# Kernel tuning notes

Measured on AMD Instinct MI355X. Metric: run time of the kernel, lower is better.

Reference implementation:

```python
import jax, jax.numpy as jnp
import numpy as np
import math

N_HEADS = 8
EMB = 128
KEY_DIM = EMB // N_HEADS  # 16
B, NQ, T = 32, 1024, 1024


def _uniform(key, shape, stdv):
    return jax.random.uniform(key, shape, jnp.float32, -stdv, stdv)


def setup_inputs() -> dict:
    key = jax.random.key(0)
    ks = jax.random.split(key, 7)
    stdv = 1.0 / math.sqrt(KEY_DIM)      # last dim of w_query/w_key/w_value
    stdv_o = 1.0 / math.sqrt(EMB)        # last dim of w_out
    q = jax.random.normal(ks[0], (B, NQ, EMB), jnp.float32)
    h = jax.random.normal(ks[1], (B, T, EMB), jnp.float32)
    mask = jax.random.randint(ks[2], (B, NQ, T), 0, 2).astype(bool)
    return {
        "q": q,
        "h": h,
        "mask": mask,
        "w_query": _uniform(ks[3], (N_HEADS, EMB, KEY_DIM), stdv),
        "w_key": _uniform(ks[4], (N_HEADS, EMB, KEY_DIM), stdv),
        "w_value": _uniform(ks[5], (N_HEADS, EMB, KEY_DIM), stdv),
        "w_out": _uniform(ks[6], (N_HEADS, KEY_DIM, EMB), stdv_o),
    }


def reference(q, h, mask, w_query, w_key, w_value, w_out):
    # q: [B, NQ, E], h: [B, T, E], mask: [B, NQ, T] (True = blocked)
    scale = 1.0 / math.sqrt(KEY_DIM)
    Q = jnp.einsum('bqi,hik->hbqk', q, w_query)   # [H,B,NQ,dk]
    K = jnp.einsum('bti,hik->hbtk', h, w_key)     # [H,B,T,dk]
    V = jnp.einsum('bti,hiv->hbtv', h, w_value)   # [H,B,T,dv]
    U = scale * jnp.einsum('hbqk,hbtk->hbqt', Q, K)  # [H,B,NQ,T]
    m = mask[None]                                   # broadcast over heads
    U = jnp.where(m, -jnp.inf, U)
    attn = jax.nn.softmax(U, axis=-1)
    attn = jnp.where(m, 0.0, attn)                   # explicit zeroing as in original
    heads = jnp.einsum('hbqt,hbtv->hbqv', attn, V)   # [H,B,NQ,dv]
    out = jnp.einsum('hbqv,hve->bqe', heads, w_out)  # [B,NQ,E]
    return out
```

## Files before the change

kernel.cpp:

```cpp
#include <hip/hip_runtime.h>
#include <hip/hip_bf16.h>
#include <stdint.h>


typedef __attribute__((ext_vector_type(8))) short bf16x8;
typedef __attribute__((ext_vector_type(4))) float f32x4;

#define NEGBIG (-1e30f)
#define QSCALE 0.36067376022224085f
#define EXP2(x) __builtin_amdgcn_exp2f(x)

__device__ __forceinline__ unsigned short f2bf(float x) {
  union { __hip_bfloat16 h; unsigned short u; } cv;
  cv.h = __float2bfloat16(x);
  return cv.u;
}
__device__ __forceinline__ unsigned int pk2bf(float a, float b) {
  unsigned int ua = __float_as_uint(a) + 0x8000u;
  unsigned int ub = __float_as_uint(b) + 0x8000u;
  return __builtin_amdgcn_perm(ub, ua, 0x07060302u);
}

__global__ __launch_bounds__(256) void maskpack_k(const void* __restrict__ mask,
                                                  unsigned long long* __restrict__ mp64) {
  __shared__ unsigned short mlds[256];
  const int tid = threadIdx.x;
  const unsigned int* mi = (const unsigned int*)mask;
  unsigned int acc = 0;
  #pragma unroll
  for (int k = 0; k < 16; ++k) acc |= mi[k * 251];
  const bool bytemode = acc > 1u;

  const long long i0 = ((long long)blockIdx.x * 256 + tid) * 16;
  unsigned int v = 0;
  if (bytemode) {
    int4 w = *(const int4*)((const unsigned char*)mask + i0);
    unsigned int ws[4] = {(unsigned)w.x, (unsigned)w.y, (unsigned)w.z, (unsigned)w.w};
    #pragma unroll
    for (int d = 0; d < 4; ++d)
      #pragma unroll
      for (int j = 0; j < 4; ++j)
        v |= (((ws[d] >> (8*j)) & 0xFFu) ? 1u : 0u) << (d*4 + j);
  } else {
    const int4* mp = (const int4*)((const int*)mask + i0);
    #pragma unroll
    for (int d = 0; d < 4; ++d) {
      int4 w = mp[d];
      v |= (w.x ? 1u : 0u) << (d*4 + 0);
      v |= (w.y ? 1u : 0u) << (d*4 + 1);
      v |= (w.z ? 1u : 0u) << (d*4 + 2);
      v |= (w.w ? 1u : 0u) << (d*4 + 3);
    }
  }
  mlds[tid] = (unsigned short)v;
  __syncthreads();
  if (tid < 64)
    mp64[(long long)blockIdx.x * 64 + tid] = ((const unsigned long long*)mlds)[tid];
}

__global__ __launch_bounds__(256) void projqkv_k(const float* __restrict__ qp,
                                                 const float* __restrict__ hp,
                                                 const float* __restrict__ wqp,
                                                 const float* __restrict__ wkp,
                                                 const float* __restrict__ wvp,
                                                 unsigned short* __restrict__ Qb,
                                                 unsigned short* __restrict__ Kb,
                                                 unsigned short* __restrict__ Vt) {
  __shared__ unsigned short WtLds[128 * 136];
  __shared__ __align__(16) unsigned short Cxf[9216];
  const int tid = threadIdx.x;
  const int wave = tid >> 6, lane = tid & 63;
  const int llo4 = lane & 15, lhi4 = lane >> 4;
  const int m0 = blockIdx.x * 64;
  const int b = m0 >> 10, row0 = m0 & 1023;
  const int sel = blockIdx.y;
  const float* A = (sel == 0) ? qp : hp;
  const float* W = (sel == 0) ? wqp : (sel == 1) ? wkp : wvp;
  const float wscale = (sel == 0) ? QSCALE : 1.0f;

  #pragma unroll
  for (int i = 0; i < 8; ++i) {
    int base = (tid + i * 256) * 8;
    float4 w0 = *(const float4*)&W[base];
    float4 w1 = *(const float4*)&W[base + 4];
    float wv8[8] = {w0.x, w0.y, w0.z, w0.w, w1.x, w1.y, w1.z, w1.w};
    #pragma unroll
    for (int j = 0; j < 8; ++j) {
      int idx = base + j;
      int h = idx >> 11, e = (idx >> 4) & 127, kk = idx & 15;
      WtLds[(h*16 + kk) * 136 + e] = f2bf(wv8[j] * wscale);
    }
  }
  #pragma unroll
  for (int i = 0; i < 4; ++i) {
    int r = (tid >> 4) + i * 16;
    int c = (tid & 15) * 8;
    float4 a0 = *(const float4*)&A[(m0 + r) * 128 + c];
    float4 a1 = *(const float4*)&A[(m0 + r) * 128 + c + 4];
    bf16x8 a8;
    a8[0] = (short)f2bf(a0.x); a8[1] = (short)f2bf(a0.y);
    a8[2] = (short)f2bf(a0.z); a8[3] = (short)f2bf(a0.w);
    a8[4] = (short)f2bf(a1.x); a8[5] = (short)f2bf(a1.y);
    a8[6] = (short)f2bf(a1.z); a8[7] = (short)f2bf(a1.w);
    *(bf16x8*)&Cxf[r * 136 + c] = a8;
  }
  __syncthreads();

  const int n0 = wave * 32;
  f32x4 acc[4][2] = {};
  #pragma unroll
  for (int kk = 0; kk < 128; kk += 32) {
    bf16x8 af[4], bfr[2];
    #pragma unroll
    for (int mi2 = 0; mi2 < 4; ++mi2)
      af[mi2] = *(const bf16x8*)&Cxf[(mi2*16 + llo4)*136 + kk + lhi4*8];
    #pragma unroll
    for (int ni = 0; ni < 2; ++ni)
      bfr[ni] = *(const bf16x8*)&WtLds[(n0 + ni*16 + llo4)*136 + kk + lhi4*8];
    #pragma unroll
    for (int mi2 = 0; mi2 < 4; ++mi2)
      #pragma unroll
      for (int ni = 0; ni < 2; ++ni)
        acc[mi2][ni] = __builtin_amdgcn_mfma_f32_16x16x32_bf16(af[mi2], bfr[ni], acc[mi2][ni], 0, 0, 0);
  }

  __syncthreads();
  if (sel < 2) {
    unsigned short* Cb = sel ? Kb : Qb;
    #pragma unroll
    for (int mi2 = 0; mi2 < 4; ++mi2)
      #pragma unroll
      for (int ni = 0; ni < 2; ++ni) {
        int n = n0 + ni*16 + llo4;
        #pragma unroll
        for (int r = 0; r < 4; ++r)
          Cxf[(mi2*16 + lhi4*4 + r)*136 + n] = f2bf(acc[mi2][ni][r]);
      }
    __syncthreads();
    #pragma unroll
    for (int it = 0; it < 4; ++it) {
      int u = tid + it*256;
      int h = u >> 7, rk = u & 127, row = rk >> 1, kh = rk & 1;
      bf16x8 vv = *(const bf16x8*)&Cxf[row*136 + h*16 + kh*8];
      *(bf16x8*)&Cb[((b*8 + h)*1024 + row0 + row)*16 + kh*8] = vv;
    }
  } else {
    #pragma unroll
    for (int mi2 = 0; mi2 < 4; ++mi2)
      #pragma unroll
      for (int ni = 0; ni < 2; ++ni) {
        int n = n0 + ni*16 + llo4;
        ushort4 pk;
        pk.x = f2bf(acc[mi2][ni][0]); pk.y = f2bf(acc[mi2][ni][1]);
        pk.z = f2bf(acc[mi2][ni][2]); pk.w = f2bf(acc[mi2][ni][3]);
        *(ushort4*)&Cxf[n*72 + mi2*16 + lhi4*4] = pk;
      }
    __syncthreads();
    #pragma unroll
    for (int it = 0; it < 4; ++it) {
      int u = tid + it*256;
      int n = u >> 3, tc = u & 7;
      int h = n >> 4, k = n & 15;
      bf16x8 vv = *(const bf16x8*)&Cxf[n*72 + tc*8];
      *(bf16x8*)&Vt[((b*8 + h)*16 + k)*1024 + row0 + tc*8] = vv;
    }
  }
}

__global__ __launch_bounds__(256) void attn_k(const unsigned short* __restrict__ Qb,
                                              const unsigned short* __restrict__ Kb,
                                              const unsigned short* __restrict__ Vtb,
                                              const unsigned long long* __restrict__ mp64,
                                              unsigned short* __restrict__ heads) {
  __shared__ __align__(16) unsigned short Plds[4][16 * 72];
  const int tid = threadIdx.x;
  const int wave = tid >> 6, lane = tid & 63;
  const int llo4 = lane & 15, lhi4 = lane >> 4;
  const int q0 = blockIdx.x * 64 + wave * 16;
  const int b  = blockIdx.y;
  const int h  = blockIdx.z;
  const int bh = b * 8 + h;
  unsigned short* Pw = &Plds[wave][0];
  const unsigned long long* mrow_p = &mp64[((b << 10) + q0 + llo4) * 16];

  bf16x8 qf = {};
  if (lhi4 < 2)
    qf = *(const bf16x8*)&Qb[(bh * 1024 + q0 + llo4) * 16 + lhi4 * 8];

  bf16x8 kf[4] = {};
  bf16x8 ones;
  #pragma unroll
  for (int j = 0; j < 8; ++j) ones[j] = (short)0x3F80;
  const f32x4 cbias = {-18.f, -18.f, -18.f, -18.f};

  f32x4 ot = {};
  f32x4 lacc = {};

  for (int tw = 0; tw < 16; ++tw) {
    const int t0 = tw * 64;
    if (lhi4 < 2) {
      #pragma unroll
      for (int tt = 0; tt < 4; ++tt)
        kf[tt] = *(const bf16x8*)&Kb[(bh * 1024 + t0 + tt*16 + llo4) * 16 + lhi4 * 8];
    }
    bf16x8 vf[2];
    #pragma unroll
    for (int kt = 0; kt < 2; ++kt)
      vf[kt] = *(const bf16x8*)&Vtb[(bh * 16 + llo4) * 1024 + t0 + kt*32 + lhi4 * 8];
    unsigned long long mw = mrow_p[tw];

    f32x4 st[4];
    #pragma unroll
    for (int tt = 0; tt < 4; ++tt)
      st[tt] = __builtin_amdgcn_mfma_f32_16x16x32_bf16(kf[tt], qf, cbias, 0, 0, 0);

    #pragma unroll
    for (int tt = 0; tt < 4; ++tt) {
      unsigned int msh = (unsigned int)(mw >> (tt*16 + lhi4*4));
      #pragma unroll
      for (int r = 0; r < 4; ++r) {
        float s = ((msh >> r) & 1u) ? NEGBIG : st[tt][r];
        st[tt][r] = EXP2(s);
      }
    }
    #pragma unroll
    for (int tt = 0; tt < 4; ++tt) {
      uint2 d;
      d.x = pk2bf(st[tt][0], st[tt][1]);
      d.y = pk2bf(st[tt][2], st[tt][3]);
      *(uint2*)&Pw[llo4 * 72 + tt*16 + lhi4*4] = d;
    }
    #pragma unroll
    for (int kt = 0; kt < 2; ++kt) {
      bf16x8 pf = *(const bf16x8*)&Pw[llo4 * 72 + kt*32 + lhi4*8];
      ot   = __builtin_amdgcn_mfma_f32_16x16x32_bf16(vf[kt], pf, ot, 0, 0, 0);
      lacc = __builtin_amdgcn_mfma_f32_16x16x32_bf16(ones,  pf, lacc, 0, 0, 0);
    }
  }

  float l = lacc[0];
  float inv = l > 0.f ? 1.f / l : 0.f;
  f32x4 o = ot * inv;
  uint2 d;
  d.x = pk2bf(o[0], o[1]);
  d.y = pk2bf(o[2], o[3]);
  *(uint2*)&heads[((b << 10) + q0 + llo4) * 128 + h*16 + lhi4*4] = d;
}

__global__ __launch_bounds__(256) void outproj_k(const unsigned short* __restrict__ Av,
                                                 const float* __restrict__ W,
                                                 float* __restrict__ Co) {
  __shared__ unsigned short WtLds[128 * 136];
  __shared__ __align__(16) unsigned short Cxf[9216];
  const int tid = threadIdx.x;
  const int wave = tid >> 6, lane = tid & 63;
  const int llo4 = lane & 15, lhi4 = lane >> 4;
  const int m0 = blockIdx.x * 64;

  #pragma unroll
  for (int i = 0; i < 8; ++i) {
    int base = (tid + i * 256) * 8;
    float4 w0 = *(const float4*)&W[base];
    float4 w1 = *(const float4*)&W[base + 4];
    float wv8[8] = {w0.x, w0.y, w0.z, w0.w, w1.x, w1.y, w1.z, w1.w};
    #pragma unroll
    for (int j = 0; j < 8; ++j) {
      int idx = base + j;
      WtLds[(idx & 127) * 136 + (idx >> 7)] = f2bf(wv8[j]);
    }
  }
  #pragma unroll
  for (int i = 0; i < 4; ++i) {
    int r = (tid >> 4) + i * 16;
    int c = (tid & 15) * 8;
    *(bf16x8*)&Cxf[r * 136 + c] = *(const bf16x8*)&Av[(m0 + r) * 128 + c];
  }
  __syncthreads();

  const int n0 = wave * 32;
  f32x4 acc[4][2] = {};
  #pragma unroll
  for (int kk = 0; kk < 128; kk += 32) {
    bf16x8 af[4], bfr[2];
    #pragma unroll
    for (int mi2 = 0; mi2 < 4; ++mi2)
      af[mi2] = *(const bf16x8*)&Cxf[(mi2*16 + llo4)*136 + kk + lhi4*8];
    #pragma unroll
    for (int ni = 0; ni < 2; ++ni)
      bfr[ni] = *(const bf16x8*)&WtLds[(n0 + ni*16 + llo4)*136 + kk + lhi4*8];
    #pragma unroll
    for (int mi2 = 0; mi2 < 4; ++mi2)
      #pragma unroll
      for (int ni = 0; ni < 2; ++ni)
        acc[mi2][ni] = __builtin_amdgcn_mfma_f32_16x16x32_bf16(af[mi2], bfr[ni], acc[mi2][ni], 0, 0, 0);
  }
  #pragma unroll
  for (int mi2 = 0; mi2 < 4; ++mi2)
    #pragma unroll
    for (int ni = 0; ni < 2; ++ni) {
      int n = n0 + ni*16 + llo4;
      int mbase = m0 + mi2*16 + lhi4*4;
      #pragma unroll
      for (int r = 0; r < 4; ++r)
        Co[(mbase + r) * 128 + n] = acc[mi2][ni][r];
    }
}

extern "C" void kernel_launch(void* const* d_in, const int* in_sizes, int n_in,
                              void* d_out, int out_size, void* d_ws, size_t ws_size,
                              hipStream_t stream) {
  const float* q  = (const float*)d_in[0];
  const float* hh = (const float*)d_in[1];
  const void*  mk = d_in[2];
  const float* wq = (const float*)d_in[3];
  const float* wk = (const float*)d_in[4];
  const float* wv = (const float*)d_in[5];
  const float* wo = (const float*)d_in[6];
  float* out = (float*)d_out;

  unsigned short* Qb = (unsigned short*)d_ws;
  unsigned short* Kb = Qb + 32*8*1024*16;
  unsigned short* Vt = Kb + 32*8*1024*16;
  unsigned short* hd = Vt + 32*8*1024*16;
  unsigned long long* mp64 = (unsigned long long*)(hd + 32768*128);

  maskpack_k<<<8192, 256, 0, stream>>>(mk, mp64);
  projqkv_k<<<dim3(512, 3), 256, 0, stream>>>(q, hh, wq, wk, wv, Qb, Kb, Vt);
  attn_k<<<dim3(16, 32, 8), 256, 0, stream>>>(Qb, Kb, Vt, mp64, hd);
  outproj_k<<<512, 256, 0, stream>>>(hd, wo, out);
}
```

Measured before the change: 361.1 us.

## Process two query tiles per wave and prefetch next K/V/mask tile

```diff
diff --git a/kernel.cpp b/kernel.cpp
--- a/kernel.cpp
+++ b/kernel.cpp
@@ -172,79 +172,116 @@
                                               const unsigned short* __restrict__ Vtb,
                                               const unsigned long long* __restrict__ mp64,
                                               unsigned short* __restrict__ heads) {
-  __shared__ __align__(16) unsigned short Plds[4][16 * 72];
+  __shared__ __align__(16) unsigned short Plds[4][32 * 72];
   const int tid = threadIdx.x;
   const int wave = tid >> 6, lane = tid & 63;
   const int llo4 = lane & 15, lhi4 = lane >> 4;
-  const int q0 = blockIdx.x * 64 + wave * 16;
+  const int q0 = blockIdx.x * 128 + wave * 32;
   const int b  = blockIdx.y;
   const int h  = blockIdx.z;
   const int bh = b * 8 + h;
   unsigned short* Pw = &Plds[wave][0];
-  const unsigned long long* mrow_p = &mp64[((b << 10) + q0 + llo4) * 16];
-
-  bf16x8 qf = {};
-  if (lhi4 < 2)
-    qf = *(const bf16x8*)&Qb[(bh * 1024 + q0 + llo4) * 16 + lhi4 * 8];
-
-  bf16x8 kf[4] = {};
+  const unsigned long long* mp_base = &mp64[((b << 10) + q0 + llo4) * 16];
+  const unsigned short* Kbase = &Kb[(bh * 1024 + llo4) * 16 + lhi4 * 8];
+  const unsigned short* Vbase = &Vtb[(bh * 16 + llo4) * 1024 + lhi4 * 8];
+
+  bf16x8 qf[2];
+  #pragma unroll
+  for (int qn = 0; qn < 2; ++qn) {
+    bf16x8 z = {};
+    if (lhi4 < 2)
+      z = *(const bf16x8*)&Qb[(bh * 1024 + q0 + qn*16 + llo4) * 16 + lhi4 * 8];
+    qf[qn] = z;
+  }
+
   bf16x8 ones;
   #pragma unroll
   for (int j = 0; j < 8; ++j) ones[j] = (short)0x3F80;
   const f32x4 cbias = {-18.f, -18.f, -18.f, -18.f};
 
-  f32x4 ot = {};
-  f32x4 lacc = {};
+  f32x4 ot[2] = {};
+  f32x4 lacc[2] = {};
+
+  bf16x8 kfc[4] = {}, kfn[4] = {};
+  bf16x8 vfc[2], vfn[2];
+  unsigned long long mwc[2], mwn[2];
+
+  if (lhi4 < 2) {
+    #pragma unroll
+    for (int tt = 0; tt < 4; ++tt)
+      kfc[tt] = *(const bf16x8*)&Kbase[(tt*16) * 16];
+  }
+  #pragma unroll
+  for (int kt = 0; kt < 2; ++kt)
+    vfc[kt] = *(const bf16x8*)&Vbase[kt*32];
+  mwc[0] = mp_base[0];
+  mwc[1] = mp_base[256];
 
   for (int tw = 0; tw < 16; ++tw) {
-    const int t0 = tw * 64;
+    const int twn = (tw < 15) ? tw + 1 : 15;
+    const int t0n = twn * 64;
     if (lhi4 < 2) {
       #pragma unroll
       for (int tt = 0; tt < 4; ++tt)
-        kf[tt] = *(const bf16x8*)&Kb[(bh * 1024 + t0 + tt*16 + llo4) * 16 + lhi4 * 8];
-    }
-    bf16x8 vf[2];
+        kfn[tt] = *(const bf16x8*)&Kbase[(t0n + tt*16) * 16];
+    }
     #pragma unroll
     for (int kt = 0; kt < 2; ++kt)
-      vf[kt] = *(const bf16x8*)&Vtb[(bh * 16 + llo4) * 1024 + t0 + kt*32 + lhi4 * 8];
-    unsigned long long mw = mrow_p[tw];
-
-    f32x4 st[4];
+      vfn[kt] = *(const bf16x8*)&Vbase[t0n + kt*32];
+    mwn[0] = mp_base[twn];
+    mwn[1] = mp_base[256 + twn];
+
+    f32x4 st[2][4];
     #pragma unroll
     for (int tt = 0; tt < 4; ++tt)
-      st[tt] = __builtin_amdgcn_mfma_f32_16x16x32_bf16(kf[tt], qf, cbias, 0, 0, 0);
-
-    #pragma unroll
-    for (int tt = 0; tt < 4; ++tt) {
-      unsigned int msh = (unsigned int)(mw >> (tt*16 + lhi4*4));
-      #pragma unroll
-      for (int r = 0; r < 4; ++r) {
-        float s = ((msh >> r) & 1u) ? NEGBIG : st[tt][r];
-        st[tt][r] = EXP2(s);
+      #pragma unroll
+      for (int qn = 0; qn < 2; ++qn)
+        st[qn][tt] = __builtin_amdgcn_mfma_f32_16x16x32_bf16(kfc[tt], qf[qn], cbias, 0, 0, 0);
+
+    #pragma unroll
+    for (int qn = 0; qn < 2; ++qn) {
+      unsigned long long mw = mwc[qn];
+      #pragma unroll
+      for (int tt = 0; tt < 4; ++tt) {
+        unsigned int msh = (unsigned int)(mw >> (tt*16 + lhi4*4));
+        #pragma unroll
+        for (int r = 0; r < 4; ++r) {
+          float s = ((msh >> r) & 1u) ? NEGBIG : st[qn][tt][r];
+          st[qn][tt][r] = EXP2(s);
+        }
+        uint2 d;
+        d.x = pk2bf(st[qn][tt][0], st[qn][tt][1]);
+        d.y = pk2bf(st[qn][tt][2], st[qn][tt][3]);
+        *(uint2*)&Pw[(qn*16 + llo4) * 72 + tt*16 + lhi4*4] = d;
       }
     }
-    #pragma unroll
-    for (int tt = 0; tt < 4; ++tt) {
-      uint2 d;
-      d.x = pk2bf(st[tt][0], st[tt][1]);
-      d.y = pk2bf(st[tt][2], st[tt][3]);
-      *(uint2*)&Pw[llo4 * 72 + tt*16 + lhi4*4] = d;
-    }
+
     #pragma unroll
     for (int kt = 0; kt < 2; ++kt) {
-      bf16x8 pf = *(const bf16x8*)&Pw[llo4 * 72 + kt*32 + lhi4*8];
-      ot   = __builtin_amdgcn_mfma_f32_16x16x32_bf16(vf[kt], pf, ot, 0, 0, 0);
-      lacc = __builtin_amdgcn_mfma_f32_16x16x32_bf16(ones,  pf, lacc, 0, 0, 0);
-    }
-  }
-
-  float l = lacc[0];
-  float inv = l > 0.f ? 1.f / l : 0.f;
-  f32x4 o = ot * inv;
-  uint2 d;
-  d.x = pk2bf(o[0], o[1]);
-  d.y = pk2bf(o[2], o[3]);
-  *(uint2*)&heads[((b << 10) + q0 + llo4) * 128 + h*16 + lhi4*4] = d;
+      #pragma unroll
+      for (int qn = 0; qn < 2; ++qn) {
+        bf16x8 pf = *(const bf16x8*)&Pw[(qn*16 + llo4) * 72 + kt*32 + lhi4*8];
+        ot[qn]   = __builtin_amdgcn_mfma_f32_16x16x32_bf16(vfc[kt], pf, ot[qn], 0, 0, 0);
+        lacc[qn] = __builtin_amdgcn_mfma_f32_16x16x32_bf16(ones,   pf, lacc[qn], 0, 0, 0);
+      }
+    }
+
+    #pragma unroll
+    for (int tt = 0; tt < 4; ++tt) kfc[tt] = kfn[tt];
+    vfc[0] = vfn[0]; vfc[1] = vfn[1];
+    mwc[0] = mwn[0]; mwc[1] = mwn[1];
+  }
+
+  #pragma unroll
+  for (int qn = 0; qn < 2; ++qn) {
+    float l = lacc[qn][0];
+    float inv = l > 0.f ? 1.f / l : 0.f;
+    f32x4 o = ot[qn] * inv;
+    uint2 d;
+    d.x = pk2bf(o[0], o[1]);
+    d.y = pk2bf(o[2], o[3]);
+    *(uint2*)&heads[((b << 10) + q0 + qn*16 + llo4) * 128 + h*16 + lhi4*4] = d;
+  }
 }
 
 __global__ __launch_bounds__(256) void outproj_k(const unsigned short* __restrict__ Av,
@@ -326,6 +363,6 @@
 
   maskpack_k<<<8192, 256, 0, stream>>>(mk, mp64);
   projqkv_k<<<dim3(512, 3), 256, 0, stream>>>(q, hh, wq, wk, wv, Qb, Kb, Vt);
-  attn_k<<<dim3(16, 32, 8), 256, 0, stream>>>(Qb, Kb, Vt, mp64, hd);
+  attn_k<<<dim3(8, 32, 8), 256, 0, stream>>>(Qb, Kb, Vt, mp64, hd);
   outproj_k<<<512, 256, 0, stream>>>(hd, wo, out);
 }
```

After: 328.9 us. 8.9% less time.
